# Kernel tuning notes

Measured on AMD Instinct MI355X. Metric: run time of the kernel, lower is better.

Reference implementation:

```python
import jax, jax.numpy as jnp
import numpy as np

B, S, D, H, L, V = 2, 2048, 1024, 16, 4, 2000
DK = D // H
DFF = 4 * D
EPS = 1e-5


def _pos_encoding(s, d):
    pos = np.arange(s, dtype=np.float64)[:, None]
    i = np.arange(d, dtype=np.float64)[None, :]
    angle = pos / np.power(10000.0, (i - (i % 2)) / d)
    pe = np.where(i % 2 == 0, np.sin(angle), np.cos(angle))
    return jnp.asarray(pe, jnp.float32)  # [S, D]


def setup_inputs() -> dict:
    key = jax.random.key(0)
    ks = jax.random.split(key, 12)
    sc = 0.02
    return {
        "indices": jax.random.randint(ks[0], (B, S), 0, V),
        "emb": jax.random.normal(ks[1], (V, D), jnp.float32) * sc,
        "Wq": jax.random.normal(ks[2], (L, H, DK, D), jnp.float32) * sc,
        "Wk": jax.random.normal(ks[3], (L, H, DK, D), jnp.float32) * sc,
        "Wv": jax.random.normal(ks[4], (L, H, DK, D), jnp.float32) * sc,
        "Wo": jax.random.normal(ks[5], (L, D, D), jnp.float32) * sc,
        "ln1_w": jnp.ones((L, D), jnp.float32),
        "ln1_b": jnp.zeros((L, D), jnp.float32),
        "W1": jax.random.normal(ks[6], (L, DFF, D), jnp.float32) * sc,
        "W2": jax.random.normal(ks[7], (L, D, DFF), jnp.float32) * sc,
        "ln2_w": jnp.ones((L, D), jnp.float32),
        "ln2_b": jnp.zeros((L, D), jnp.float32),
        "Wout": jax.random.normal(ks[8], (V, D), jnp.float32) * sc,
    }


def _layernorm(x, w, b):
    m = jnp.mean(x, axis=-1, keepdims=True)
    v = jnp.mean(jnp.square(x - m), axis=-1, keepdims=True)
    return (x - m) * jax.lax.rsqrt(v + EPS) * w + b


def reference(indices, emb, Wq, Wk, Wv, Wo, ln1_w, ln1_b, W1, W2, ln2_w, ln2_b, Wout):
    x = emb[indices] + _pos_encoding(S, D)  # [B, S, D]
    causal = jnp.tril(jnp.ones((S, S), bool))
    inv_sqrt_dk = 1.0 / np.sqrt(DK)
    for l in range(L):
        # per-head QKV projections, vectorized over heads
        q = jnp.einsum("bsd,hkd->bhsk", x, Wq[l])
        k = jnp.einsum("bsd,hkd->bhsk", x, Wk[l])
        v = jnp.einsum("bsd,hkd->bhsk", x, Wv[l])
        scores = jnp.einsum("bhqk,bhmk->bhqm", q, k) * inv_sqrt_dk
        scores = jnp.where(causal, scores, -jnp.inf)
        attn = jax.nn.softmax(scores, axis=-1)
        o = jnp.einsum("bhqm,bhmk->bhqk", attn, v)
        o = o.transpose(0, 2, 1, 3).reshape(B, S, D)  # concat heads
        o = o @ Wo[l].T
        x = _layernorm(x + o, ln1_w[l], ln1_b[l])
        h = jax.nn.relu(x @ W1[l].T) @ W2[l].T
        x = _layernorm(x + h, ln2_w[l], ln2_b[l])
    return x @ Wout.T  # [B, S, V]
```

## Files before the change

kernel.cpp:

```cpp
#include <hip/hip_runtime.h>
#include <hip/hip_bf16.h>

#define B_   2
#define S_   2048
#define D_   1024
#define H_   16
#define L_   4
#define DK_  64
#define DFF_ 4096
#define V_   2000

typedef __bf16 bf16x8 __attribute__((ext_vector_type(8)));
typedef float  f32x4  __attribute__((ext_vector_type(4)));
typedef __attribute__((address_space(1))) const void* as1cv;
typedef __attribute__((address_space(3))) void* as3v;

__device__ __forceinline__ void async_copy16(const void* g, void* l) {
    __builtin_amdgcn_global_load_lds((as1cv)g, (as3v)l, 16, 0, 0);
}

__global__ __launch_bounds__(256)
void canon_k(const void* __restrict__ src, __hip_bfloat16* __restrict__ dst,
             long n, const unsigned short* __restrict__ probe)
{
    const bool isbf = (probe[0] == 0x3F80u);
    long i0 = ((long)blockIdx.x * 256 + threadIdx.x) * 8;
    if (isbf) {
        const __hip_bfloat16* s = (const __hip_bfloat16*)src;
        #pragma unroll
        for (int j = 0; j < 8; ++j) {
            long i = i0 + j;
            if (i < n) dst[i] = s[i];
        }
    } else {
        const float* s = (const float*)src;
        #pragma unroll
        for (int j = 0; j < 8; ++j) {
            long i = i0 + j;
            if (i < n) dst[i] = __float2bfloat16(s[i]);
        }
    }
}

template<int MODE>
__global__ __launch_bounds__(256, 2)
void gemm_bt(const __hip_bfloat16* __restrict__ A,
             const __hip_bfloat16* __restrict__ Wa,
             const __hip_bfloat16* __restrict__ Wb,
             const __hip_bfloat16* __restrict__ Wc,
             void* __restrict__ Oa, void* __restrict__ Obp, void* __restrict__ Ocp,
             const __hip_bfloat16* __restrict__ Res,
             const unsigned short* __restrict__ probe,
             int M, int N, int K)
{
    const __hip_bfloat16* W = Wa;
    void* Out = Oa;
    if (blockIdx.z == 1) { W = Wb; Out = Obp; }
    else if (blockIdx.z == 2) { W = Wc; Out = Ocp; }

    __shared__ __bf16 As[2][128 * 32];
    __shared__ __bf16 Bs[2][128 * 32];

    const int tid  = threadIdx.x;
    const int wave = tid >> 6;
    const int lane = tid & 63;
    const int quad = lane >> 4;
    const int l16  = lane & 15;
    const int bm = blockIdx.x;
    const int bn = blockIdx.y;
    const int wm = (wave >> 1) * 64;
    const int wn = (wave & 1) * 64;

    const int sr = tid >> 2;
    const int sc = (tid & 3) * 8;
    const __hip_bfloat16* ap0 = A + (long)(bm * 128 + sr) * K + sc;
    const __hip_bfloat16* ap1 = ap0 + (long)64 * K;
    const __hip_bfloat16* bp0 = W + (long)(bn * 128 + sr) * K + sc;
    const __hip_bfloat16* bp1 = bp0 + (long)64 * K;
    const bool bok0 = (bn * 128 + sr) < N;
    const bool bok1 = (bn * 128 + sr + 64) < N;

    if (N & 127) {
        #pragma unroll
        for (int bi = 0; bi < 2; ++bi)
            #pragma unroll
            for (int j = 0; j < 2; ++j)
                *(bf16x8*)(Bs[bi] + (j * 256 + tid) * 8) = (bf16x8)0;
        __syncthreads();
    }

    f32x4 acc[4][4] = {};
    const int nsteps = K >> 5;

    async_copy16(ap0, As[0] + wave * 512);
    async_copy16(ap1, As[0] + 2048 + wave * 512);
    if (bok0) async_copy16(bp0, Bs[0] + wave * 512);
    if (bok1) async_copy16(bp1, Bs[0] + 2048 + wave * 512);
    __syncthreads();

    int cur = 0;
    for (int t = 0; t < nsteps; ++t) {
        const int nxt = cur ^ 1;
        if (t + 1 < nsteps) {
            const int k0 = (t + 1) << 5;
            async_copy16(ap0 + k0, As[nxt] + wave * 512);
            async_copy16(ap1 + k0, As[nxt] + 2048 + wave * 512);
            if (bok0) async_copy16(bp0 + k0, Bs[nxt] + wave * 512);
            if (bok1) async_copy16(bp1 + k0, Bs[nxt] + 2048 + wave * 512);
        }

        bf16x8 af[4], bfr[4];
        #pragma unroll
        for (int i = 0; i < 4; ++i)
            af[i] = *(const bf16x8*)(As[cur] + (wm + i * 16 + l16) * 32 + quad * 8);
        #pragma unroll
        for (int i = 0; i < 4; ++i)
            bfr[i] = *(const bf16x8*)(Bs[cur] + (wn + i * 16 + l16) * 32 + quad * 8);
        #pragma unroll
        for (int i = 0; i < 4; ++i)
            #pragma unroll
            for (int j = 0; j < 4; ++j)
                acc[i][j] = __builtin_amdgcn_mfma_f32_16x16x32_bf16(af[i], bfr[j], acc[i][j], 0, 0, 0);

        __syncthreads();
        cur = nxt;
    }

    const bool out_bf = (MODE != 1) && (MODE != 3 || probe[0] == 0x3F80u);
    #pragma unroll
    for (int i = 0; i < 4; ++i) {
        #pragma unroll
        for (int r = 0; r < 4; ++r) {
            const long row = bm * 128 + wm + i * 16 + quad * 4 + r;
            #pragma unroll
            for (int j = 0; j < 4; ++j) {
                const int col = bn * 128 + wn + j * 16 + l16;
                if (col < N) {
                    const long idx = row * (long)N + col;
                    float v = acc[i][j][r];
                    if constexpr (MODE == 1) {
                        ((float*)Out)[idx] = v + __bfloat162float(Res[idx]);
                    } else if constexpr (MODE == 2) {
                        ((__hip_bfloat16*)Out)[idx] = __float2bfloat16(v > 0.f ? v : 0.f);
                    } else {
                        if (out_bf) ((__hip_bfloat16*)Out)[idx] = __float2bfloat16(v);
                        else        ((float*)Out)[idx] = v;
                    }
                }
            }
        }
    }
}

__global__ __launch_bounds__(256, 2)
void flash_attn(const __hip_bfloat16* __restrict__ Qg,
                const __hip_bfloat16* __restrict__ Kg,
                const __hip_bfloat16* __restrict__ Vg,
                __hip_bfloat16* __restrict__ Og)
{
    const int h  = blockIdx.y;
    const int b  = blockIdx.z;
    const int tid  = threadIdx.x;
    const int wave = tid >> 6;
    const int lane = tid & 63;
    const int quad = lane >> 4;
    const int l16  = lane & 15;

    __shared__ __bf16 Qs[64 * 64];
    __shared__ __bf16 Ks[64 * 64];
    __shared__ __bf16 Vs[64 * 64];
    __shared__ __bf16 Vt[64 * 72];
    __shared__ __bf16 Ps[4][16 * 72];

    const long base = ((long)b * S_) * D_ + (long)h * DK_;
    const int sr  = tid >> 3;
    const int scq = ((tid & 7) ^ (sr & 7)) * 8;
    const int scv = (tid & 7) * 8;

    const float scale = 0.125f;

    for (int pr = 0; pr < 2; ++pr) {
        const int qt = pr ? (31 - (int)blockIdx.x) : (int)blockIdx.x;

        const __hip_bfloat16* qp = Qg + base + (long)(qt * 64 + sr) * D_ + scq;
        async_copy16(qp,           Qs + wave * 512);
        async_copy16(qp + 32 * D_, Qs + 2048 + wave * 512);
        __syncthreads();

        const int qr = wave * 16 + l16;
        const __bf16* qrow = Qs + qr * 64;
        const bf16x8 qf0 = *(const bf16x8*)(qrow + (( quad      ^ (qr & 7)) * 8));
        const bf16x8 qf1 = *(const bf16x8*)(qrow + (((quad + 4) ^ (qr & 7)) * 8));

        f32x4 o_acc[4] = {};
        float m_run[4], l_run[4];
        #pragma unroll
        for (int r = 0; r < 4; ++r) { m_run[r] = -1e30f; l_run[r] = 0.f; }

        const int q_base = qt * 64 + wave * 16 + quad * 4;

        for (int kv0 = 0; kv0 <= qt * 64; kv0 += 64) {
            const __hip_bfloat16* kp = Kg + base + (long)(kv0 + sr) * D_ + scq;
            const __hip_bfloat16* vp = Vg + base + (long)(kv0 + sr) * D_ + scv;
            async_copy16(kp,           Ks + wave * 512);
            async_copy16(kp + 32 * D_, Ks + 2048 + wave * 512);
            async_copy16(vp,           Vs + wave * 512);
            async_copy16(vp + 32 * D_, Vs + 2048 + wave * 512);
            __syncthreads();

            #pragma unroll
            for (int i = 0; i < 2; ++i) {
                const int seg = i * 256 + tid;
                const int dk  = seg & 63;
                const int kvc = (seg >> 6) * 8;
                bf16x8 t;
                #pragma unroll
                for (int j = 0; j < 8; ++j) t[j] = Vs[(kvc + j) * 64 + dk];
                *(bf16x8*)(Vt + dk * 72 + kvc) = t;
            }
            __syncthreads();

            f32x4 sAcc[4] = {};
            #pragma unroll
            for (int nt = 0; nt < 4; ++nt) {
                const int kr = nt * 16 + l16;
                const __bf16* krow = Ks + kr * 64;
                const bf16x8 kf0 = *(const bf16x8*)(krow + (( quad      ^ (kr & 7)) * 8));
                const bf16x8 kf1 = *(const bf16x8*)(krow + (((quad + 4) ^ (kr & 7)) * 8));
                sAcc[nt] = __builtin_amdgcn_mfma_f32_16x16x32_bf16(qf0, kf0, sAcc[nt], 0, 0, 0);
                sAcc[nt] = __builtin_amdgcn_mfma_f32_16x16x32_bf16(qf1, kf1, sAcc[nt], 0, 0, 0);
            }

            const bool diag = (kv0 == qt * 64);
            float rmax[4];
            #pragma unroll
            for (int r = 0; r < 4; ++r) rmax[r] = -1e30f;
            #pragma unroll
            for (int nt = 0; nt < 4; ++nt)
                #pragma unroll
                for (int r = 0; r < 4; ++r) {
                    float s = sAcc[nt][r] * scale;
                    if (diag && (kv0 + nt * 16 + l16) > (q_base + r)) s = -1e30f;
                    sAcc[nt][r] = s;
                    rmax[r] = fmaxf(rmax[r], s);
                }
            #pragma unroll
            for (int off = 1; off < 16; off <<= 1)
                #pragma unroll
                for (int r = 0; r < 4; ++r)
                    rmax[r] = fmaxf(rmax[r], __shfl_xor(rmax[r], off, 64));

            float alpha[4], rsum[4];
            #pragma unroll
            for (int r = 0; r < 4; ++r) {
                const float mn = fmaxf(m_run[r], rmax[r]);
                alpha[r] = __expf(m_run[r] - mn);
                m_run[r] = mn;
                rsum[r] = 0.f;
            }
            #pragma unroll
            for (int nt = 0; nt < 4; ++nt)
                #pragma unroll
                for (int r = 0; r < 4; ++r) {
                    const float p = __expf(sAcc[nt][r] - m_run[r]);
                    sAcc[nt][r] = p;
                    rsum[r] += p;
                }
            #pragma unroll
            for (int off = 1; off < 16; off <<= 1)
                #pragma unroll
                for (int r = 0; r < 4; ++r)
                    rsum[r] += __shfl_xor(rsum[r], off, 64);
            #pragma unroll
            for (int r = 0; r < 4; ++r) l_run[r] = l_run[r] * alpha[r] + rsum[r];
            #pragma unroll
            for (int nt = 0; nt < 4; ++nt)
                #pragma unroll
                for (int r = 0; r < 4; ++r) o_acc[nt][r] *= alpha[r];

            __bf16* pw = &Ps[wave][0];
            #pragma unroll
            for (int nt = 0; nt < 4; ++nt)
                #pragma unroll
                for (int r = 0; r < 4; ++r)
                    pw[(quad * 4 + r) * 72 + nt * 16 + l16] = (__bf16)sAcc[nt][r];
            __syncthreads();
            const __bf16* pb = pw + l16 * 72 + quad * 8;
            const bf16x8 pf0 = *(const bf16x8*)pb;
            const bf16x8 pf1 = *(const bf16x8*)(pb + 32);
            #pragma unroll
            for (int nt = 0; nt < 4; ++nt) {
                const __bf16* vb = Vt + (nt * 16 + l16) * 72 + quad * 8;
                o_acc[nt] = __builtin_amdgcn_mfma_f32_16x16x32_bf16(pf0, *(const bf16x8*)vb,        o_acc[nt], 0, 0, 0);
                o_acc[nt] = __builtin_amdgcn_mfma_f32_16x16x32_bf16(pf1, *(const bf16x8*)(vb + 32), o_acc[nt], 0, 0, 0);
            }
            __syncthreads();
        }

        #pragma unroll
        for (int nt = 0; nt < 4; ++nt)
            #pragma unroll
            for (int r = 0; r < 4; ++r) {
                const long row = (long)b * S_ + qt * 64 + wave * 16 + quad * 4 + r;
                const int col = h * DK_ + nt * 16 + l16;
                Og[row * D_ + col] = __float2bfloat16(o_acc[nt][r] / l_run[r]);
            }
    }
}

__global__ __launch_bounds__(256)
void layernorm_k(const float* __restrict__ in,
                 const __hip_bfloat16* __restrict__ w,
                 const __hip_bfloat16* __restrict__ bb,
                 __hip_bfloat16* __restrict__ out)
{
    const int row = blockIdx.x;
    const int tid = threadIdx.x;
    const float4 v = ((const float4*)(in + (long)row * D_))[tid];
    float s  = v.x + v.y + v.z + v.w;
    float ss = v.x * v.x + v.y * v.y + v.z * v.z + v.w * v.w;
    #pragma unroll
    for (int off = 1; off < 64; off <<= 1) {
        s  += __shfl_xor(s, off, 64);
        ss += __shfl_xor(ss, off, 64);
    }
    __shared__ float red[8];
    if ((tid & 63) == 0) { red[tid >> 6] = s; red[4 + (tid >> 6)] = ss; }
    __syncthreads();
    s  = red[0] + red[1] + red[2] + red[3];
    ss = red[4] + red[5] + red[6] + red[7];
    const float mean = s * (1.f / D_);
    const float var  = ss * (1.f / D_) - mean * mean;
    const float rs = rsqrtf(var + 1e-5f);
    const int d0 = tid * 4;
    const float xs[4] = { v.x, v.y, v.z, v.w };
    #pragma unroll
    for (int j = 0; j < 4; ++j) {
        const float wv = __bfloat162float(w[d0 + j]);
        const float bv = __bfloat162float(bb[d0 + j]);
        out[(long)row * D_ + d0 + j] = __float2bfloat16((xs[j] - mean) * rs * wv + bv);
    }
}

__global__ __launch_bounds__(256)
void embed_k(const int* __restrict__ idx,
             const __hip_bfloat16* __restrict__ emb,
             __hip_bfloat16* __restrict__ X)
{
    const int row = blockIdx.x;
    const int s = row & (S_ - 1);
    const int tid = threadIdx.x;
    const int token = idx[row];
    const __hip_bfloat16* e = emb + (long)token * D_;
    #pragma unroll
    for (int j = 0; j < 4; ++j) {
        const int d = tid + j * 256;
        const float di = (float)(d & ~1);
        const float freq = __expf(di * (-9.210340371976184f / (float)D_));
        const float angle = (float)s * freq;
        const float pe = (d & 1) ? cosf(angle) : sinf(angle);
        X[(long)row * D_ + d] = __float2bfloat16(__bfloat162float(e[d]) + pe);
    }
}

extern "C" void kernel_launch(void* const* d_in, const int* in_sizes, int n_in,
                              void* d_out, int out_size, void* d_ws, size_t ws_size,
                              hipStream_t stream)
{
    const int* indices = (const int*)d_in[0];
    const unsigned short* probe = (const unsigned short*)d_in[6];

    const long NTOK = (long)B_ * S_;
    char* ws = (char*)d_ws;
    __hip_bfloat16* X  = (__hip_bfloat16*)ws; ws += NTOK * D_ * 2;
    __hip_bfloat16* Qb = (__hip_bfloat16*)ws; ws += NTOK * D_ * 2;
    __hip_bfloat16* Kb = (__hip_bfloat16*)ws; ws += NTOK * D_ * 2;
    __hip_bfloat16* Vb = (__hip_bfloat16*)ws; ws += NTOK * D_ * 2;
    __hip_bfloat16* Ob = (__hip_bfloat16*)ws; ws += NTOK * D_ * 2;
    __hip_bfloat16* Hb = Qb;
    float* tmp = (float*)ws;                  ws += NTOK * D_ * 4;
    __hip_bfloat16* cEmb  = (__hip_bfloat16*)ws; ws += (long)V_ * D_ * 2;
    __hip_bfloat16* cWq   = (__hip_bfloat16*)ws; ws += (long)L_ * D_ * D_ * 2;
    __hip_bfloat16* cWk   = (__hip_bfloat16*)ws; ws += (long)L_ * D_ * D_ * 2;
    __hip_bfloat16* cWv   = (__hip_bfloat16*)ws; ws += (long)L_ * D_ * D_ * 2;
    __hip_bfloat16* cWo   = (__hip_bfloat16*)ws; ws += (long)L_ * D_ * D_ * 2;
    __hip_bfloat16* cW1   = (__hip_bfloat16*)ws; ws += (long)L_ * DFF_ * D_ * 2;
    __hip_bfloat16* cW2   = (__hip_bfloat16*)ws; ws += (long)L_ * D_ * DFF_ * 2;
    __hip_bfloat16* cWout = (__hip_bfloat16*)ws; ws += (long)V_ * D_ * 2;
    __hip_bfloat16* cLn1w = (__hip_bfloat16*)ws; ws += (long)L_ * D_ * 2;
    __hip_bfloat16* cLn1b = (__hip_bfloat16*)ws; ws += (long)L_ * D_ * 2;
    __hip_bfloat16* cLn2w = (__hip_bfloat16*)ws; ws += (long)L_ * D_ * 2;
    __hip_bfloat16* cLn2b = (__hip_bfloat16*)ws; ws += (long)L_ * D_ * 2;

    struct { const void* src; __hip_bfloat16* dst; long n; } cv[12] = {
        { d_in[1],  cEmb,  (long)V_ * D_ },
        { d_in[2],  cWq,   (long)L_ * D_ * D_ },
        { d_in[3],  cWk,   (long)L_ * D_ * D_ },
        { d_in[4],  cWv,   (long)L_ * D_ * D_ },
        { d_in[5],  cWo,   (long)L_ * D_ * D_ },
        { d_in[6],  cLn1w, (long)L_ * D_ },
        { d_in[7],  cLn1b, (long)L_ * D_ },
        { d_in[8],  cW1,   (long)L_ * DFF_ * D_ },
        { d_in[9],  cW2,   (long)L_ * D_ * DFF_ },
        { d_in[10], cLn2w, (long)L_ * D_ },
        { d_in[11], cLn2b, (long)L_ * D_ },
        { d_in[12], cWout, (long)V_ * D_ },
    };
    for (int i = 0; i < 12; ++i) {
        const long blocks = (cv[i].n + 2047) / 2048;
        canon_k<<<dim3((unsigned)blocks), 256, 0, stream>>>(cv[i].src, cv[i].dst, cv[i].n, probe);
    }

    embed_k<<<dim3(NTOK), 256, 0, stream>>>(indices, cEmb, X);

    for (int l = 0; l < L_; ++l) {
        const __hip_bfloat16* wq = cWq + (long)l * D_ * D_;
        const __hip_bfloat16* wk = cWk + (long)l * D_ * D_;
        const __hip_bfloat16* wv = cWv + (long)l * D_ * D_;
        const __hip_bfloat16* wo = cWo + (long)l * D_ * D_;
        const __hip_bfloat16* w1 = cW1 + (long)l * DFF_ * D_;
        const __hip_bfloat16* w2 = cW2 + (long)l * D_ * DFF_;

        gemm_bt<0><<<dim3(32, 8, 3), 256, 0, stream>>>(X, wq, wk, wv, Qb, Kb, Vb, nullptr, nullptr, 4096, 1024, 1024);
        flash_attn<<<dim3(16, 16, 2), 256, 0, stream>>>(Qb, Kb, Vb, Ob);
        gemm_bt<1><<<dim3(32, 8, 1), 256, 0, stream>>>(Ob, wo, wo, wo, tmp, tmp, tmp, X, nullptr, 4096, 1024, 1024);
        layernorm_k<<<dim3(4096), 256, 0, stream>>>(tmp, cLn1w + l * D_, cLn1b + l * D_, X);
        gemm_bt<2><<<dim3(32, 32, 1), 256, 0, stream>>>(X, w1, w1, w1, Hb, Hb, Hb, nullptr, nullptr, 4096, 4096, 1024);
        gemm_bt<1><<<dim3(32, 8, 1), 256, 0, stream>>>(Hb, w2, w2, w2, tmp, tmp, tmp, X, nullptr, 4096, 1024, 4096);
        layernorm_k<<<dim3(4096), 256, 0, stream>>>(tmp, cLn2w + l * D_, cLn2b + l * D_, X);
    }

    gemm_bt<3><<<dim3(32, 16, 1), 256, 0, stream>>>(X, cWout, cWout, cWout, d_out, d_out, d_out, nullptr, probe, 4096, V_, 1024);
}
```

Baseline: 1.615 ms.

## Double-buffer K/V tiles in flash attention and use narrower GEMM tiles

Flash attention now keeps two K/V shared-memory buffers and prefetches the next KV tile while the current one is processed. This also removes one barrier per iteration, so global load latency can overlap with the MFMA and softmax work. Separately, the GEMM gains a BN template parameter, and the two N=1024 residual GEMMs (Wo and W2) now run with 64-wide N tiles. That doubles their block count to fill the GPU better, at the cost of less B-operand reuse per block. Extra LDS use in attention may reduce occupancy.

```diff
diff --git a/kernel.cpp b/kernel.cpp
--- a/kernel.cpp
+++ b/kernel.cpp
@@ -42,7 +42,7 @@
     }
 }
 
-template<int MODE>
+template<int MODE, int BN = 128>
 __global__ __launch_bounds__(256, 2)
 void gemm_bt(const __hip_bfloat16* __restrict__ A,
              const __hip_bfloat16* __restrict__ Wa,
@@ -53,13 +53,15 @@
              const unsigned short* __restrict__ probe,
              int M, int N, int K)
 {
+    constexpr int NFR = BN / 32;
+
     const __hip_bfloat16* W = Wa;
     void* Out = Oa;
     if (blockIdx.z == 1) { W = Wb; Out = Obp; }
     else if (blockIdx.z == 2) { W = Wc; Out = Ocp; }
 
     __shared__ __bf16 As[2][128 * 32];
-    __shared__ __bf16 Bs[2][128 * 32];
+    __shared__ __bf16 Bs[2][BN * 32];
 
     const int tid  = threadIdx.x;
     const int wave = tid >> 6;
@@ -69,33 +71,32 @@
     const int bm = blockIdx.x;
     const int bn = blockIdx.y;
     const int wm = (wave >> 1) * 64;
-    const int wn = (wave & 1) * 64;
+    const int wn = (wave & 1) * (BN / 2);
 
     const int sr = tid >> 2;
     const int sc = (tid & 3) * 8;
     const __hip_bfloat16* ap0 = A + (long)(bm * 128 + sr) * K + sc;
     const __hip_bfloat16* ap1 = ap0 + (long)64 * K;
-    const __hip_bfloat16* bp0 = W + (long)(bn * 128 + sr) * K + sc;
+    const __hip_bfloat16* bp0 = W + (long)(bn * BN + sr) * K + sc;
     const __hip_bfloat16* bp1 = bp0 + (long)64 * K;
-    const bool bok0 = (bn * 128 + sr) < N;
-    const bool bok1 = (bn * 128 + sr + 64) < N;
-
-    if (N & 127) {
+    const bool bok0 = (bn * BN + sr) < N;
+    const bool bok1 = (BN == 128) && (bn * BN + sr + 64) < N;
+
+    if (N % BN) {
         #pragma unroll
         for (int bi = 0; bi < 2; ++bi)
-            #pragma unroll
-            for (int j = 0; j < 2; ++j)
-                *(bf16x8*)(Bs[bi] + (j * 256 + tid) * 8) = (bf16x8)0;
+            for (int c = tid; c < BN * 4; c += 256)
+                ((bf16x8*)Bs[bi])[c] = (bf16x8)0;
         __syncthreads();
     }
 
-    f32x4 acc[4][4] = {};
+    f32x4 acc[4][NFR] = {};
     const int nsteps = K >> 5;
 
     async_copy16(ap0, As[0] + wave * 512);
     async_copy16(ap1, As[0] + 2048 + wave * 512);
     if (bok0) async_copy16(bp0, Bs[0] + wave * 512);
-    if (bok1) async_copy16(bp1, Bs[0] + 2048 + wave * 512);
+    if constexpr (BN == 128) { if (bok1) async_copy16(bp1, Bs[0] + 2048 + wave * 512); }
     __syncthreads();
 
     int cur = 0;
@@ -106,20 +107,20 @@
             async_copy16(ap0 + k0, As[nxt] + wave * 512);
             async_copy16(ap1 + k0, As[nxt] + 2048 + wave * 512);
             if (bok0) async_copy16(bp0 + k0, Bs[nxt] + wave * 512);
-            if (bok1) async_copy16(bp1 + k0, Bs[nxt] + 2048 + wave * 512);
-        }
-
-        bf16x8 af[4], bfr[4];
+            if constexpr (BN == 128) { if (bok1) async_copy16(bp1 + k0, Bs[nxt] + 2048 + wave * 512); }
+        }
+
+        bf16x8 af[4], bfr[NFR];
         #pragma unroll
         for (int i = 0; i < 4; ++i)
             af[i] = *(const bf16x8*)(As[cur] + (wm + i * 16 + l16) * 32 + quad * 8);
         #pragma unroll
+        for (int i = 0; i < NFR; ++i)
+            bfr[i] = *(const bf16x8*)(Bs[cur] + (wn + i * 16 + l16) * 32 + quad * 8);
+        #pragma unroll
         for (int i = 0; i < 4; ++i)
-            bfr[i] = *(const bf16x8*)(Bs[cur] + (wn + i * 16 + l16) * 32 + quad * 8);
-        #pragma unroll
-        for (int i = 0; i < 4; ++i)
-            #pragma unroll
-            for (int j = 0; j < 4; ++j)
+            #pragma unroll
+            for (int j = 0; j < NFR; ++j)
                 acc[i][j] = __builtin_amdgcn_mfma_f32_16x16x32_bf16(af[i], bfr[j], acc[i][j], 0, 0, 0);
 
         __syncthreads();
@@ -133,8 +134,8 @@
         for (int r = 0; r < 4; ++r) {
             const long row = bm * 128 + wm + i * 16 + quad * 4 + r;
             #pragma unroll
-            for (int j = 0; j < 4; ++j) {
-                const int col = bn * 128 + wn + j * 16 + l16;
+            for (int j = 0; j < NFR; ++j) {
+                const int col = bn * BN + wn + j * 16 + l16;
                 if (col < N) {
                     const long idx = row * (long)N + col;
                     float v = acc[i][j][r];
@@ -167,8 +168,8 @@
     const int l16  = lane & 15;
 
     __shared__ __bf16 Qs[64 * 64];
-    __shared__ __bf16 Ks[64 * 64];
-    __shared__ __bf16 Vs[64 * 64];
+    __shared__ __bf16 Ks[2][64 * 64];
+    __shared__ __bf16 Vs[2][64 * 64];
     __shared__ __bf16 Vt[64 * 72];
     __shared__ __bf16 Ps[4][16 * 72];
 
@@ -181,10 +182,19 @@
 
     for (int pr = 0; pr < 2; ++pr) {
         const int qt = pr ? (31 - (int)blockIdx.x) : (int)blockIdx.x;
+        const int ntile = qt + 1;
 
         const __hip_bfloat16* qp = Qg + base + (long)(qt * 64 + sr) * D_ + scq;
         async_copy16(qp,           Qs + wave * 512);
         async_copy16(qp + 32 * D_, Qs + 2048 + wave * 512);
+        {
+            const __hip_bfloat16* kp = Kg + base + (long)sr * D_ + scq;
+            const __hip_bfloat16* vp = Vg + base + (long)sr * D_ + scv;
+            async_copy16(kp,           Ks[0] + wave * 512);
+            async_copy16(kp + 32 * D_, Ks[0] + 2048 + wave * 512);
+            async_copy16(vp,           Vs[0] + wave * 512);
+            async_copy16(vp + 32 * D_, Vs[0] + 2048 + wave * 512);
+        }
         __syncthreads();
 
         const int qr = wave * 16 + l16;
@@ -199,14 +209,19 @@
 
         const int q_base = qt * 64 + wave * 16 + quad * 4;
 
-        for (int kv0 = 0; kv0 <= qt * 64; kv0 += 64) {
-            const __hip_bfloat16* kp = Kg + base + (long)(kv0 + sr) * D_ + scq;
-            const __hip_bfloat16* vp = Vg + base + (long)(kv0 + sr) * D_ + scv;
-            async_copy16(kp,           Ks + wave * 512);
-            async_copy16(kp + 32 * D_, Ks + 2048 + wave * 512);
-            async_copy16(vp,           Vs + wave * 512);
-            async_copy16(vp + 32 * D_, Vs + 2048 + wave * 512);
-            __syncthreads();
+        for (int it = 0; it < ntile; ++it) {
+            const int cur = it & 1;
+            const int kv0 = it * 64;
+
+            if (it + 1 < ntile) {
+                const int nxt = cur ^ 1;
+                const __hip_bfloat16* kp = Kg + base + (long)(kv0 + 64 + sr) * D_ + scq;
+                const __hip_bfloat16* vp = Vg + base + (long)(kv0 + 64 + sr) * D_ + scv;
+                async_copy16(kp,           Ks[nxt] + wave * 512);
+                async_copy16(kp + 32 * D_, Ks[nxt] + 2048 + wave * 512);
+                async_copy16(vp,           Vs[nxt] + wave * 512);
+                async_copy16(vp + 32 * D_, Vs[nxt] + 2048 + wave * 512);
+            }
 
             #pragma unroll
             for (int i = 0; i < 2; ++i) {
@@ -215,16 +230,15 @@
                 const int kvc = (seg >> 6) * 8;
                 bf16x8 t;
                 #pragma unroll
-                for (int j = 0; j < 8; ++j) t[j] = Vs[(kvc + j) * 64 + dk];
+                for (int j = 0; j < 8; ++j) t[j] = Vs[cur][(kvc + j) * 64 + dk];
                 *(bf16x8*)(Vt + dk * 72 + kvc) = t;
             }
-            __syncthreads();
 
             f32x4 sAcc[4] = {};
             #pragma unroll
             for (int nt = 0; nt < 4; ++nt) {
                 const int kr = nt * 16 + l16;
-                const __bf16* krow = Ks + kr * 64;
+                const __bf16* krow = Ks[cur] + kr * 64;
                 const bf16x8 kf0 = *(const bf16x8*)(krow + (( quad      ^ (kr & 7)) * 8));
                 const bf16x8 kf1 = *(const bf16x8*)(krow + (((quad + 4) ^ (kr & 7)) * 8));
                 sAcc[nt] = __builtin_amdgcn_mfma_f32_16x16x32_bf16(qf0, kf0, sAcc[nt], 0, 0, 0);
@@ -284,7 +298,9 @@
                 #pragma unroll
                 for (int r = 0; r < 4; ++r)
                     pw[(quad * 4 + r) * 72 + nt * 16 + l16] = (__bf16)sAcc[nt][r];
+
             __syncthreads();
+
             const __bf16* pb = pw + l16 * 72 + quad * 8;
             const bf16x8 pf0 = *(const bf16x8*)pb;
             const bf16x8 pf1 = *(const bf16x8*)(pb + 32);
@@ -294,6 +310,7 @@
                 o_acc[nt] = __builtin_amdgcn_mfma_f32_16x16x32_bf16(pf0, *(const bf16x8*)vb,        o_acc[nt], 0, 0, 0);
                 o_acc[nt] = __builtin_amdgcn_mfma_f32_16x16x32_bf16(pf1, *(const bf16x8*)(vb + 32), o_acc[nt], 0, 0, 0);
             }
+
             __syncthreads();
         }
 
@@ -423,10 +440,10 @@
 
         gemm_bt<0><<<dim3(32, 8, 3), 256, 0, stream>>>(X, wq, wk, wv, Qb, Kb, Vb, nullptr, nullptr, 4096, 1024, 1024);
         flash_attn<<<dim3(16, 16, 2), 256, 0, stream>>>(Qb, Kb, Vb, Ob);
-        gemm_bt<1><<<dim3(32, 8, 1), 256, 0, stream>>>(Ob, wo, wo, wo, tmp, tmp, tmp, X, nullptr, 4096, 1024, 1024);
+        gemm_bt<1, 64><<<dim3(32, 16, 1), 256, 0, stream>>>(Ob, wo, wo, wo, tmp, tmp, tmp, X, nullptr, 4096, 1024, 1024);
         layernorm_k<<<dim3(4096), 256, 0, stream>>>(tmp, cLn1w + l * D_, cLn1b + l * D_, X);
         gemm_bt<2><<<dim3(32, 32, 1), 256, 0, stream>>>(X, w1, w1, w1, Hb, Hb, Hb, nullptr, nullptr, 4096, 4096, 1024);
-        gemm_bt<1><<<dim3(32, 8, 1), 256, 0, stream>>>(Hb, w2, w2, w2, tmp, tmp, tmp, X, nullptr, 4096, 1024, 4096);
+        gemm_bt<1, 64><<<dim3(32, 16, 1), 256, 0, stream>>>(Hb, w2, w2, w2, tmp, tmp, tmp, X, nullptr, 4096, 1024, 4096);
         layernorm_k<<<dim3(4096), 256, 0, stream>>>(tmp, cLn2w + l * D_, cLn2b + l * D_, X);
     }
 
```

Result: faster. 1.531 ms (-5.2%).
